# Kernel optimization log

Measured on AMD Instinct MI355X. Metric: run time of the kernel, lower is better.

## Reference

```python
import jax, jax.numpy as jnp
import numpy as np

B, N, D, OC, STEPS = 4096, 64, 128, 64, 3


def _xavier(k, shape):
    limit = float(np.sqrt(6.0 / (shape[0] + shape[1])))
    return jax.random.uniform(k, shape, jnp.float32, -limit, limit)


def setup_inputs() -> dict:
    key = jax.random.key(0)
    ks = jax.random.split(key, 14)
    u = 1.0 / float(np.sqrt(D))  # torch GRUCell/Linear default init range
    return {
        "h": jax.random.normal(ks[0], (B, N, D), jnp.float32),
        "adj": jax.random.normal(ks[1], (B, N, N), jnp.float32),
        "a_src": _xavier(ks[2], (D, 1)),
        "a_dst": _xavier(ks[3], (D, 1)),
        "w": _xavier(ks[4], (D, D)),
        "bias": jnp.zeros((D,), jnp.float32),
        "W_ih": jax.random.uniform(ks[5], (3 * D, D), jnp.float32, -u, u),
        "W_hh": jax.random.uniform(ks[6], (3 * D, D), jnp.float32, -u, u),
        "b_ih": jax.random.uniform(ks[7], (3 * D,), jnp.float32, -u, u),
        "b_hh": jax.random.uniform(ks[8], (3 * D,), jnp.float32, -u, u),
        "mlp1_w": jax.random.uniform(ks[9], (D, OC), jnp.float32, -u, u),
        "mlp1_b": jax.random.uniform(ks[10], (OC,), jnp.float32, -u, u),
        "mlp2_w": jax.random.uniform(ks[11], (D, 1), jnp.float32, -u, u),
        "mlp2_b": jax.random.uniform(ks[12], (1,), jnp.float32, -u, u),
        "steps": STEPS,
    }


def _gru_cell(x, hprev, W_ih, W_hh, b_ih, b_hh):
    # torch.nn.GRUCell math; x, hprev: (..., D)
    gi = x @ W_ih.T + b_ih        # (..., 3D)
    gh = hprev @ W_hh.T + b_hh    # (..., 3D)
    i_r, i_z, i_n = jnp.split(gi, 3, axis=-1)
    h_r, h_z, h_n = jnp.split(gh, 3, axis=-1)
    r = jax.nn.sigmoid(i_r + h_r)
    z = jax.nn.sigmoid(i_z + h_z)
    n = jnp.tanh(i_n + r * h_n)
    return (1.0 - z) * n + z * hprev


def reference(h, adj, a_src, a_dst, w, bias, W_ih, W_hh, b_ih, b_hh,
              mlp1_w, mlp1_b, mlp2_w, mlp2_b, steps):
    n = adj.shape[-1]
    attn_src = h @ a_src                      # (B, N, 1)
    attn_dst = h @ a_dst                      # (B, N, 1)
    attn = attn_src + jnp.swapaxes(attn_dst, 1, 2)   # (B, N, N) outer-sum
    attn = jax.nn.leaky_relu(attn, negative_slope=0.2)
    mask = 1.0 - jnp.eye(n, dtype=attn.dtype)        # zero the diagonal (as in source)
    attn = jax.nn.softmax(attn * mask, axis=-1)

    s = h
    for _ in range(int(steps)):
        a = jnp.einsum('bij,bjd->bid', attn, s @ w) + bias   # message passing
        s = _gru_cell(a, s, W_ih, W_hh, b_ih, b_hh)           # pointwise GRU update
        s = s + h                                             # residual connection

    output = s @ mlp1_w + mlp1_b              # (B, N, OC)
    weight = s @ mlp2_w + mlp2_b              # (B, N, 1)
    out = jnp.einsum('bni,bnc->bic', weight, output)  # (B, 1, OC)
    return jnp.squeeze(out, axis=1)           # (B, OC)
```

## Files before the change

kernel.cpp:

```cpp
#include <hip/hip_runtime.h>
#include <hip/hip_bf16.h>

typedef unsigned short u16t;
typedef __attribute__((ext_vector_type(8))) short bf16x8;
typedef __attribute__((ext_vector_type(4))) float f32x4;

__device__ __forceinline__ float bf2f(u16t u) {
  union { unsigned int i; float f; } v; v.i = ((unsigned int)u) << 16; return v.f;
}
__device__ __forceinline__ float bitsf(unsigned int u) {
  union { unsigned int i; float f; } v; v.i = u; return v.f;
}
__device__ __forceinline__ u16t f2bf(float f) {
  union { float f; unsigned int i; } v; v.f = f;
  return (u16t)((v.i + 0x7fffu + ((v.i >> 16) & 1u)) >> 16);
}
__device__ __forceinline__ unsigned int cvtpk(float lo, float hi) {
  float2 f; f.x = lo; f.y = hi;
  __hip_bfloat162 b = __float22bfloat162_rn(f);
  unsigned int r; __builtin_memcpy(&r, &b, 4); return r;
}
__device__ __forceinline__ float frcp(float x) { return __builtin_amdgcn_rcpf(x); }
__device__ __forceinline__ float sigm(float x) { return frcp(1.0f + __expf(-x)); }
__device__ __forceinline__ float tanh_f(float x) { return 1.0f - 2.0f * frcp(__expf(2.0f * x) + 1.0f); }
__device__ __forceinline__ float lrelu(float x) { return x > 0.0f ? x : 0.2f * x; }

__device__ __forceinline__ float ldf(const void* p, long i, bool isbf) {
  return isbf ? bf2f(((const u16t*)p)[i]) : ((const float*)p)[i];
}
__device__ __forceinline__ bf16x8 ld8(const void* p, long i, bool isbf) {
  if (isbf) return *reinterpret_cast<const bf16x8*>((const u16t*)p + i);
  const float* f = (const float*)p + i;
  bf16x8 r;
  #pragma unroll
  for (int j = 0; j < 8; ++j) r[j] = (short)f2bf(f[j]);
  return r;
}
__device__ __forceinline__ bool sniff_bf(const void* h_g) {
  bool isbf = true;
  #pragma unroll
  for (int i = 0; i < 16; ++i) {
    u16t u = ((const u16t*)h_g)[2 * i];
    int e = (u >> 7) & 0xFF;
    if (e < 100 || e > 142) isbf = false;
  }
  return isbf;
}

#define MFMA16(a, b, c) __builtin_amdgcn_mfma_f32_16x16x32_bf16((a), (b), (c), 0, 0, 0)

#define DDIM 128
#define SD 136
#define ST 72
#define R0_OFF 0
#define R1_OFF 9216
#define R2_OFF 18432
#define AT_OFF 27648
#define NLDS   32256

#define WS_W_OFF   0
#define WS_IH_OFF  16384
#define WS_HH_OFF  65536
#define WS_M1_OFF  114688
#define WS_ELEMS   122880

__global__ __launch_bounds__(256) void prep(
    const void* __restrict__ h_g, const void* __restrict__ w_g,
    const void* __restrict__ wih_g, const void* __restrict__ whh_g,
    const void* __restrict__ m1w_g, u16t* __restrict__ ws) {
  const bool isbf = sniff_bf(h_g);
  const int idx = blockIdx.x * 256 + threadIdx.x;
  if (idx >= WS_ELEMS) return;
  float val;
  if (idx < WS_IH_OFF) {
    int t = idx;
    int j = t & 7, lane = (t >> 3) & 63, ks = (t >> 9) & 3, wv = t >> 11;
    val = ldf(w_g, (long)(ks * 32 + (lane >> 4) * 8 + j) * DDIM + wv * 16 + (lane & 15), isbf);
  } else if (idx < WS_HH_OFF) {
    int t = idx - WS_IH_OFF;
    int j = t & 7, lane = (t >> 3) & 63, ks = (t >> 9) & 3, rem = t >> 11;
    int g = rem % 3, wv = rem / 3;
    val = ldf(wih_g, (long)(g * 128 + wv * 16 + (lane & 15)) * DDIM + ks * 32 + (lane >> 4) * 8 + j, isbf);
  } else if (idx < WS_M1_OFF) {
    int t = idx - WS_HH_OFF;
    int j = t & 7, lane = (t >> 3) & 63, ks = (t >> 9) & 3, rem = t >> 11;
    int g = rem % 3, wv = rem / 3;
    val = ldf(whh_g, (long)(g * 128 + wv * 16 + (lane & 15)) * DDIM + ks * 32 + (lane >> 4) * 8 + j, isbf);
  } else {
    int t = idx - WS_M1_OFF;
    int j = t & 7, lane = (t >> 3) & 63, ks = (t >> 9) & 3, wv = t >> 11;
    val = ldf(m1w_g, (long)(ks * 32 + (lane >> 4) * 8 + j) * 64 + wv * 16 + (lane & 15), isbf);
  }
  ws[idx] = f2bf(val);
}

template <bool WSOK>
__global__ __launch_bounds__(512) void fignn(
    const void* __restrict__ h_g, const void* __restrict__ asrc_g,
    const void* __restrict__ adst_g, const void* __restrict__ w_g,
    const void* __restrict__ bias_g, const void* __restrict__ wih_g,
    const void* __restrict__ whh_g, const void* __restrict__ bih_g,
    const void* __restrict__ bhh_g, const void* __restrict__ m1w_g,
    const void* __restrict__ m1b_g, const void* __restrict__ m2w_g,
    const void* __restrict__ m2b_g, const int* __restrict__ steps_p,
    const u16t* __restrict__ ws_g, void* __restrict__ out_g) {
  __shared__ __align__(16) u16t lds[NLDS];
  __shared__ __align__(16) float ldsf[192];
  u16t* sh_at = lds + AT_OFF;
  float* f_src = ldsf;
  float* f_dst = ldsf + 64;
  float* f_wv  = ldsf + 128;

  const int tid  = threadIdx.x;
  const int wv   = tid >> 6;
  const int lane = tid & 63;
  const int quad = lane >> 4;
  const int lrow = lane & 15;
  const int col  = wv * 16 + lrow;
  const int b    = blockIdx.x;

  const bool isbf = sniff_bf(h_g);

  u16t* s_c = lds + R0_OFF;
  u16t* s_m = lds + R1_OFF;
  u16t* s_a = lds + R2_OFF;

  const long hb = (long)b * (64 * DDIM);
  #pragma unroll
  for (int v = 0; v < 2; ++v) {
    int e = (tid + v * 512) * 8;
    int r = e >> 7, c = e & 127;
    *reinterpret_cast<bf16x8*>(s_c + r * SD + c) = ld8(h_g, hb + e, isbf);
  }

  unsigned int sreg2[8], hreg2[8];
  #pragma unroll
  for (int mt = 0; mt < 4; ++mt) {
    #pragma unroll
    for (int half = 0; half < 2; ++half) {
      long i0 = hb + (long)(mt * 16 + quad * 4 + half * 2) * DDIM + col;
      u16t lo, hi;
      if (isbf) {
        lo = ((const u16t*)h_g)[i0];
        hi = ((const u16t*)h_g)[i0 + DDIM];
      } else {
        lo = f2bf(((const float*)h_g)[i0]);
        hi = f2bf(((const float*)h_g)[i0 + DDIM]);
      }
      unsigned int p = (unsigned int)lo | ((unsigned int)hi << 16);
      hreg2[mt * 2 + half] = p;
      sreg2[mt * 2 + half] = p;
    }
  }

  const float msg_b = ldf(bias_g, col, isbf);
  const float bsum_r = ldf(bih_g, col, isbf) + ldf(bhh_g, col, isbf);
  const float bsum_z = ldf(bih_g, 128 + col, isbf) + ldf(bhh_g, 128 + col, isbf);
  const float b_in   = ldf(bih_g, 256 + col, isbf);
  const float b_hn   = ldf(bhh_g, 256 + col, isbf);
  int steps = *steps_p;
  if (steps < 1 || steps > 64) steps = 3;
  __syncthreads();

  if (tid < 128) {
    const int node = tid >> 1, half = tid & 1;
    float sa = 0.f, da = 0.f;
    #pragma unroll
    for (int k = half * 64; k < half * 64 + 64; k += 8) {
      bf16x8 hv = *reinterpret_cast<const bf16x8*>(s_c + node * SD + k);
      #pragma unroll
      for (int j = 0; j < 8; ++j) {
        float hf = bf2f((u16t)hv[j]);
        sa += hf * ldf(asrc_g, k + j, isbf);
        da += hf * ldf(adst_g, k + j, isbf);
      }
    }
    sa += __shfl_xor(sa, 1);
    da += __shfl_xor(da, 1);
    if (half == 0) { f_src[node] = sa; f_dst[node] = da; }
  }
  __syncthreads();
  {
    const int row = tid >> 3, sub = tid & 7;
    const float si = f_src[row];
    float vals[8];
    float mx = 0.0f;
    #pragma unroll
    for (int u = 0; u < 8; ++u) {
      int j = sub + u * 8;
      float vv = (j == row) ? 0.0f : lrelu(si + f_dst[j]);
      vals[u] = vv;
      mx = fmaxf(mx, vv);
    }
    mx = fmaxf(mx, __shfl_xor(mx, 1));
    mx = fmaxf(mx, __shfl_xor(mx, 2));
    mx = fmaxf(mx, __shfl_xor(mx, 4));
    float sum = 0.f;
    #pragma unroll
    for (int u = 0; u < 8; ++u) { vals[u] = __expf(vals[u] - mx); sum += vals[u]; }
    sum += __shfl_xor(sum, 1);
    sum += __shfl_xor(sum, 2);
    sum += __shfl_xor(sum, 4);
    float inv = frcp(sum);
    #pragma unroll
    for (int u = 0; u < 8; u += 2) {
      unsigned int pk = cvtpk(vals[u] * inv, vals[u + 1] * inv);
      sh_at[row * ST + sub + u * 8] = (u16t)pk;
      sh_at[row * ST + sub + (u + 1) * 8] = (u16t)(pk >> 16);
    }
  }
  __syncthreads();

  for (int it = 0; it < steps; ++it) {
    {
      f32x4 macc[4] = {{0,0,0,0},{0,0,0,0},{0,0,0,0},{0,0,0,0}};
      #pragma unroll
      for (int ks = 0; ks < 4; ++ks) {
        bf16x8 bw;
        if constexpr (WSOK) {
          bw = *reinterpret_cast<const bf16x8*>(ws_g + WS_W_OFF + (((wv * 4 + ks) * 64 + lane) << 3));
        } else {
          #pragma unroll
          for (int j = 0; j < 8; ++j)
            bw[j] = (short)f2bf(ldf(w_g, (long)(ks * 32 + quad * 8 + j) * DDIM + col, isbf));
        }
        #pragma unroll
        for (int mt = 0; mt < 4; ++mt) {
          bf16x8 af = *reinterpret_cast<const bf16x8*>(s_c + (mt * 16 + lrow) * SD + ks * 32 + quad * 8);
          macc[mt] = MFMA16(af, bw, macc[mt]);
        }
      }
      #pragma unroll
      for (int mt = 0; mt < 4; ++mt) {
        uint2 pk2;
        pk2.x = cvtpk(macc[mt][0], macc[mt][1]);
        pk2.y = cvtpk(macc[mt][2], macc[mt][3]);
        *reinterpret_cast<uint2*>(s_m + col * ST + mt * 16 + quad * 4) = pk2;
      }
    }
    #pragma unroll
    for (int mt = 0; mt < 4; ++mt) {
      f32x4 acc = {0.f, 0.f, 0.f, 0.f};
      #pragma unroll
      for (int ks = 0; ks < 2; ++ks) {
        bf16x8 af  = *reinterpret_cast<const bf16x8*>(sh_at + (mt * 16 + lrow) * ST + ks * 32 + quad * 8);
        bf16x8 bfv = *reinterpret_cast<const bf16x8*>(s_m + col * ST + ks * 32 + quad * 8);
        acc = MFMA16(af, bfv, acc);
      }
      unsigned int p01 = cvtpk(acc[0] + msg_b, acc[1] + msg_b);
      unsigned int p23 = cvtpk(acc[2] + msg_b, acc[3] + msg_b);
      const int rb = (mt * 16 + quad * 4) * SD + col;
      s_a[rb         ] = (u16t)p01;
      s_a[rb + SD    ] = (u16t)(p01 >> 16);
      s_a[rb + 2 * SD] = (u16t)p23;
      s_a[rb + 3 * SD] = (u16t)(p23 >> 16);
    }
    __syncthreads();

    #pragma unroll
    for (int p = 0; p < 2; ++p) {
      f32x4 ar[2]  = {{0,0,0,0},{0,0,0,0}};
      f32x4 az[2]  = {{0,0,0,0},{0,0,0,0}};
      f32x4 ain[2] = {{0,0,0,0},{0,0,0,0}};
      f32x4 ahn[2] = {{0,0,0,0},{0,0,0,0}};
      #pragma unroll
      for (int ks = 0; ks < 4; ++ks) {
        bf16x8 fa[2], fh[2];
        #pragma unroll
        for (int m = 0; m < 2; ++m) {
          const int mt = p * 2 + m;
          fa[m] = *reinterpret_cast<const bf16x8*>(s_a + (mt * 16 + lrow) * SD + ks * 32 + quad * 8);
          fh[m] = *reinterpret_cast<const bf16x8*>(s_c + (mt * 16 + lrow) * SD + ks * 32 + quad * 8);
        }
        bf16x8 bw;
        if constexpr (WSOK) bw = *reinterpret_cast<const bf16x8*>(ws_g + WS_IH_OFF + ((((wv * 3 + 0) * 4 + ks) * 64 + lane) << 3));
        else bw = ld8(wih_g, (long)(0 * 128 + col) * DDIM + ks * 32 + quad * 8, isbf);
        #pragma unroll
        for (int m = 0; m < 2; ++m) ar[m] = MFMA16(fa[m], bw, ar[m]);
        if constexpr (WSOK) bw = *reinterpret_cast<const bf16x8*>(ws_g + WS_IH_OFF + ((((wv * 3 + 1) * 4 + ks) * 64 + lane) << 3));
        else bw = ld8(wih_g, (long)(1 * 128 + col) * DDIM + ks * 32 + quad * 8, isbf);
        #pragma unroll
        for (int m = 0; m < 2; ++m) az[m] = MFMA16(fa[m], bw, az[m]);
        if constexpr (WSOK) bw = *reinterpret_cast<const bf16x8*>(ws_g + WS_IH_OFF + ((((wv * 3 + 2) * 4 + ks) * 64 + lane) << 3));
        else bw = ld8(wih_g, (long)(2 * 128 + col) * DDIM + ks * 32 + quad * 8, isbf);
        #pragma unroll
        for (int m = 0; m < 2; ++m) ain[m] = MFMA16(fa[m], bw, ain[m]);
        if constexpr (WSOK) bw = *reinterpret_cast<const bf16x8*>(ws_g + WS_HH_OFF + ((((wv * 3 + 0) * 4 + ks) * 64 + lane) << 3));
        else bw = ld8(whh_g, (long)(0 * 128 + col) * DDIM + ks * 32 + quad * 8, isbf);
        #pragma unroll
        for (int m = 0; m < 2; ++m) ar[m] = MFMA16(fh[m], bw, ar[m]);
        if constexpr (WSOK) bw = *reinterpret_cast<const bf16x8*>(ws_g + WS_HH_OFF + ((((wv * 3 + 1) * 4 + ks) * 64 + lane) << 3));
        else bw = ld8(whh_g, (long)(1 * 128 + col) * DDIM + ks * 32 + quad * 8, isbf);
        #pragma unroll
        for (int m = 0; m < 2; ++m) az[m] = MFMA16(fh[m], bw, az[m]);
        if constexpr (WSOK) bw = *reinterpret_cast<const bf16x8*>(ws_g + WS_HH_OFF + ((((wv * 3 + 2) * 4 + ks) * 64 + lane) << 3));
        else bw = ld8(whh_g, (long)(2 * 128 + col) * DDIM + ks * 32 + quad * 8, isbf);
        #pragma unroll
        for (int m = 0; m < 2; ++m) ahn[m] = MFMA16(fh[m], bw, ahn[m]);
      }
      #pragma unroll
      for (int m = 0; m < 2; ++m) {
        const int mt = p * 2 + m;
        #pragma unroll
        for (int pr = 0; pr < 2; ++pr) {
          const int e0 = pr * 2, e1 = pr * 2 + 1;
          float rg0 = sigm(ar[m][e0] + bsum_r), rg1 = sigm(ar[m][e1] + bsum_r);
          float zg0 = sigm(az[m][e0] + bsum_z), zg1 = sigm(az[m][e1] + bsum_z);
          float ng0 = tanh_f(ain[m][e0] + b_in + rg0 * (ahn[m][e0] + b_hn));
          float ng1 = tanh_f(ain[m][e1] + b_in + rg1 * (ahn[m][e1] + b_hn));
          unsigned int sp = sreg2[mt * 2 + pr], hp = hreg2[mt * 2 + pr];
          float sn0 = (1.0f - zg0) * ng0 + zg0 * bitsf(sp << 16) + bitsf(hp << 16);
          float sn1 = (1.0f - zg1) * ng1 + zg1 * bitsf(sp & 0xffff0000u) + bitsf(hp & 0xffff0000u);
          unsigned int pk = cvtpk(sn0, sn1);
          sreg2[mt * 2 + pr] = pk;
          const int rb = (mt * 16 + quad * 4 + pr * 2) * SD + col;
          s_m[rb     ] = (u16t)pk;
          s_m[rb + SD] = (u16t)(pk >> 16);
        }
      }
    }
    __syncthreads();
    u16t* t = s_c; s_c = s_m; s_m = s_a; s_a = t;
  }

  f32x4 oacc[4] = {{0,0,0,0},{0,0,0,0},{0,0,0,0},{0,0,0,0}};
  if (wv < 4) {
    #pragma unroll
    for (int ks = 0; ks < 4; ++ks) {
      bf16x8 bw;
      if constexpr (WSOK) {
        bw = *reinterpret_cast<const bf16x8*>(ws_g + WS_M1_OFF + (((wv * 4 + ks) * 64 + lane) << 3));
      } else {
        #pragma unroll
        for (int j = 0; j < 8; ++j)
          bw[j] = (short)f2bf(ldf(m1w_g, (long)(ks * 32 + quad * 8 + j) * 64 + col, isbf));
      }
      #pragma unroll
      for (int mt = 0; mt < 4; ++mt) {
        bf16x8 af = *reinterpret_cast<const bf16x8*>(s_c + (mt * 16 + lrow) * SD + ks * 32 + quad * 8);
        oacc[mt] = MFMA16(af, bw, oacc[mt]);
      }
    }
    const float b1c = ldf(m1b_g, col, isbf);
    #pragma unroll
    for (int mt = 0; mt < 4; ++mt)
      #pragma unroll
      for (int r = 0; r < 4; ++r) oacc[mt][r] += b1c;
  } else if (wv == 4) {
    float acc = 0.f;
    #pragma unroll
    for (int k = 0; k < 128; k += 8) {
      bf16x8 sv = *reinterpret_cast<const bf16x8*>(s_c + lane * SD + k);
      #pragma unroll
      for (int j = 0; j < 8; ++j) acc += bf2f((u16t)sv[j]) * ldf(m2w_g, k + j, isbf);
    }
    f_wv[lane] = acc + ldf(m2b_g, 0, isbf);
  }
  __syncthreads();
  if (wv < 4) {
    float p = 0.f;
    #pragma unroll
    for (int mt = 0; mt < 4; ++mt)
      #pragma unroll
      for (int r = 0; r < 4; ++r)
        p += f_wv[mt * 16 + quad * 4 + r] * oacc[mt][r];
    p += __shfl_xor(p, 16);
    p += __shfl_xor(p, 32);
    if (quad == 0) {
      if (isbf) ((u16t*)out_g)[(long)b * 64 + col] = f2bf(p);
      else      ((float*)out_g)[(long)b * 64 + col] = p;
    }
  }
}

extern "C" void kernel_launch(void* const* d_in, const int* in_sizes, int n_in,
                              void* d_out, int out_size, void* d_ws, size_t ws_size,
                              hipStream_t stream) {
  (void)in_sizes; (void)n_in; (void)out_size;
  const bool wsok = ws_size >= (size_t)WS_ELEMS * 2;
  if (wsok) {
    prep<<<dim3((WS_ELEMS + 255) / 256), dim3(256), 0, stream>>>(
        d_in[0], d_in[4], d_in[6], d_in[7], d_in[10], (u16t*)d_ws);
    fignn<true><<<dim3(4096), dim3(512), 0, stream>>>(
        d_in[0], d_in[2], d_in[3], d_in[4], d_in[5], d_in[6], d_in[7], d_in[8],
        d_in[9], d_in[10], d_in[11], d_in[12], d_in[13], (const int*)d_in[14],
        (const u16t*)d_ws, d_out);
  } else {
    fignn<false><<<dim3(4096), dim3(512), 0, stream>>>(
        d_in[0], d_in[2], d_in[3], d_in[4], d_in[5], d_in[6], d_in[7], d_in[8],
        d_in[9], d_in[10], d_in[11], d_in[12], d_in[13], (const int*)d_in[14],
        (const u16t*)d_ws, d_out);
  }
}
```

Before: 646.7 us.

## Fuse hidden-state GRU matmuls into the message projection pass before the barrier

Computes the W_hh gate products (r, z, hn) during the s@w projection phase, reusing the same s_c A-fragments, so they run before the attention matmul and barrier rather than after. The post-barrier phase then only does the W_ih products over all four row tiles at once, with no split into two passes. The attention B-fragments are also hoisted out of the row-tile loop. This moves MFMA work off the critical path after the barrier and removes duplicate LDS reads of s_c, at the cost of keeping 12 extra accumulator vectors live across the barrier, which raises register pressure.

```diff
diff --git a/kernel.cpp b/kernel.cpp
--- a/kernel.cpp
+++ b/kernel.cpp
@@ -212,23 +212,39 @@
   __syncthreads();
 
   for (int it = 0; it < steps; ++it) {
+    f32x4 gr[4]  = {{0,0,0,0},{0,0,0,0},{0,0,0,0},{0,0,0,0}};
+    f32x4 gz[4]  = {{0,0,0,0},{0,0,0,0},{0,0,0,0},{0,0,0,0}};
+    f32x4 ghn[4] = {{0,0,0,0},{0,0,0,0},{0,0,0,0},{0,0,0,0}};
+
     {
       f32x4 macc[4] = {{0,0,0,0},{0,0,0,0},{0,0,0,0},{0,0,0,0}};
       #pragma unroll
       for (int ks = 0; ks < 4; ++ks) {
+        bf16x8 af[4];
+        #pragma unroll
+        for (int mt = 0; mt < 4; ++mt)
+          af[mt] = *reinterpret_cast<const bf16x8*>(s_c + (mt * 16 + lrow) * SD + ks * 32 + quad * 8);
         bf16x8 bw;
-        if constexpr (WSOK) {
-          bw = *reinterpret_cast<const bf16x8*>(ws_g + WS_W_OFF + (((wv * 4 + ks) * 64 + lane) << 3));
-        } else {
+        if constexpr (WSOK) bw = *reinterpret_cast<const bf16x8*>(ws_g + WS_W_OFF + (((wv * 4 + ks) * 64 + lane) << 3));
+        else {
           #pragma unroll
           for (int j = 0; j < 8; ++j)
             bw[j] = (short)f2bf(ldf(w_g, (long)(ks * 32 + quad * 8 + j) * DDIM + col, isbf));
         }
         #pragma unroll
-        for (int mt = 0; mt < 4; ++mt) {
-          bf16x8 af = *reinterpret_cast<const bf16x8*>(s_c + (mt * 16 + lrow) * SD + ks * 32 + quad * 8);
-          macc[mt] = MFMA16(af, bw, macc[mt]);
-        }
+        for (int mt = 0; mt < 4; ++mt) macc[mt] = MFMA16(af[mt], bw, macc[mt]);
+        if constexpr (WSOK) bw = *reinterpret_cast<const bf16x8*>(ws_g + WS_HH_OFF + ((((wv * 3 + 0) * 4 + ks) * 64 + lane) << 3));
+        else bw = ld8(whh_g, (long)(0 * 128 + col) * DDIM + ks * 32 + quad * 8, isbf);
+        #pragma unroll
+        for (int mt = 0; mt < 4; ++mt) gr[mt] = MFMA16(af[mt], bw, gr[mt]);
+        if constexpr (WSOK) bw = *reinterpret_cast<const bf16x8*>(ws_g + WS_HH_OFF + ((((wv * 3 + 1) * 4 + ks) * 64 + lane) << 3));
+        else bw = ld8(whh_g, (long)(1 * 128 + col) * DDIM + ks * 32 + quad * 8, isbf);
+        #pragma unroll
+        for (int mt = 0; mt < 4; ++mt) gz[mt] = MFMA16(af[mt], bw, gz[mt]);
+        if constexpr (WSOK) bw = *reinterpret_cast<const bf16x8*>(ws_g + WS_HH_OFF + ((((wv * 3 + 2) * 4 + ks) * 64 + lane) << 3));
+        else bw = ld8(whh_g, (long)(2 * 128 + col) * DDIM + ks * 32 + quad * 8, isbf);
+        #pragma unroll
+        for (int mt = 0; mt < 4; ++mt) ghn[mt] = MFMA16(af[mt], bw, ghn[mt]);
       }
       #pragma unroll
       for (int mt = 0; mt < 4; ++mt) {
@@ -238,76 +254,61 @@
         *reinterpret_cast<uint2*>(s_m + col * ST + mt * 16 + quad * 4) = pk2;
       }
     }
-    #pragma unroll
-    for (int mt = 0; mt < 4; ++mt) {
-      f32x4 acc = {0.f, 0.f, 0.f, 0.f};
-      #pragma unroll
-      for (int ks = 0; ks < 2; ++ks) {
-        bf16x8 af  = *reinterpret_cast<const bf16x8*>(sh_at + (mt * 16 + lrow) * ST + ks * 32 + quad * 8);
-        bf16x8 bfv = *reinterpret_cast<const bf16x8*>(s_m + col * ST + ks * 32 + quad * 8);
-        acc = MFMA16(af, bfv, acc);
-      }
-      unsigned int p01 = cvtpk(acc[0] + msg_b, acc[1] + msg_b);
-      unsigned int p23 = cvtpk(acc[2] + msg_b, acc[3] + msg_b);
-      const int rb = (mt * 16 + quad * 4) * SD + col;
-      s_a[rb         ] = (u16t)p01;
-      s_a[rb + SD    ] = (u16t)(p01 >> 16);
-      s_a[rb + 2 * SD] = (u16t)p23;
-      s_a[rb + 3 * SD] = (u16t)(p23 >> 16);
+    {
+      bf16x8 bfv[2];
+      #pragma unroll
+      for (int ks = 0; ks < 2; ++ks)
+        bfv[ks] = *reinterpret_cast<const bf16x8*>(s_m + col * ST + ks * 32 + quad * 8);
+      #pragma unroll
+      for (int mt = 0; mt < 4; ++mt) {
+        f32x4 acc = {0.f, 0.f, 0.f, 0.f};
+        #pragma unroll
+        for (int ks = 0; ks < 2; ++ks) {
+          bf16x8 af = *reinterpret_cast<const bf16x8*>(sh_at + (mt * 16 + lrow) * ST + ks * 32 + quad * 8);
+          acc = MFMA16(af, bfv[ks], acc);
+        }
+        unsigned int p01 = cvtpk(acc[0] + msg_b, acc[1] + msg_b);
+        unsigned int p23 = cvtpk(acc[2] + msg_b, acc[3] + msg_b);
+        const int rb = (mt * 16 + quad * 4) * SD + col;
+        s_a[rb         ] = (u16t)p01;
+        s_a[rb + SD    ] = (u16t)(p01 >> 16);
+        s_a[rb + 2 * SD] = (u16t)p23;
+        s_a[rb + 3 * SD] = (u16t)(p23 >> 16);
+      }
     }
     __syncthreads();
 
-    #pragma unroll
-    for (int p = 0; p < 2; ++p) {
-      f32x4 ar[2]  = {{0,0,0,0},{0,0,0,0}};
-      f32x4 az[2]  = {{0,0,0,0},{0,0,0,0}};
-      f32x4 ain[2] = {{0,0,0,0},{0,0,0,0}};
-      f32x4 ahn[2] = {{0,0,0,0},{0,0,0,0}};
+    {
+      f32x4 ain[4] = {{0,0,0,0},{0,0,0,0},{0,0,0,0},{0,0,0,0}};
       #pragma unroll
       for (int ks = 0; ks < 4; ++ks) {
-        bf16x8 fa[2], fh[2];
-        #pragma unroll
-        for (int m = 0; m < 2; ++m) {
-          const int mt = p * 2 + m;
-          fa[m] = *reinterpret_cast<const bf16x8*>(s_a + (mt * 16 + lrow) * SD + ks * 32 + quad * 8);
-          fh[m] = *reinterpret_cast<const bf16x8*>(s_c + (mt * 16 + lrow) * SD + ks * 32 + quad * 8);
-        }
+        bf16x8 fa[4];
+        #pragma unroll
+        for (int mt = 0; mt < 4; ++mt)
+          fa[mt] = *reinterpret_cast<const bf16x8*>(s_a + (mt * 16 + lrow) * SD + ks * 32 + quad * 8);
         bf16x8 bw;
         if constexpr (WSOK) bw = *reinterpret_cast<const bf16x8*>(ws_g + WS_IH_OFF + ((((wv * 3 + 0) * 4 + ks) * 64 + lane) << 3));
         else bw = ld8(wih_g, (long)(0 * 128 + col) * DDIM + ks * 32 + quad * 8, isbf);
         #pragma unroll
-        for (int m = 0; m < 2; ++m) ar[m] = MFMA16(fa[m], bw, ar[m]);
+        for (int mt = 0; mt < 4; ++mt) gr[mt] = MFMA16(fa[mt], bw, gr[mt]);
         if constexpr (WSOK) bw = *reinterpret_cast<const bf16x8*>(ws_g + WS_IH_OFF + ((((wv * 3 + 1) * 4 + ks) * 64 + lane) << 3));
         else bw = ld8(wih_g, (long)(1 * 128 + col) * DDIM + ks * 32 + quad * 8, isbf);
         #pragma unroll
-        for (int m = 0; m < 2; ++m) az[m] = MFMA16(fa[m], bw, az[m]);
+        for (int mt = 0; mt < 4; ++mt) gz[mt] = MFMA16(fa[mt], bw, gz[mt]);
         if constexpr (WSOK) bw = *reinterpret_cast<const bf16x8*>(ws_g + WS_IH_OFF + ((((wv * 3 + 2) * 4 + ks) * 64 + lane) << 3));
         else bw = ld8(wih_g, (long)(2 * 128 + col) * DDIM + ks * 32 + quad * 8, isbf);
         #pragma unroll
-        for (int m = 0; m < 2; ++m) ain[m] = MFMA16(fa[m], bw, ain[m]);
-        if constexpr (WSOK) bw = *reinterpret_cast<const bf16x8*>(ws_g + WS_HH_OFF + ((((wv * 3 + 0) * 4 + ks) * 64 + lane) << 3));
-        else bw = ld8(whh_g, (long)(0 * 128 + col) * DDIM + ks * 32 + quad * 8, isbf);
-        #pragma unroll
-        for (int m = 0; m < 2; ++m) ar[m] = MFMA16(fh[m], bw, ar[m]);
-        if constexpr (WSOK) bw = *reinterpret_cast<const bf16x8*>(ws_g + WS_HH_OFF + ((((wv * 3 + 1) * 4 + ks) * 64 + lane) << 3));
-        else bw = ld8(whh_g, (long)(1 * 128 + col) * DDIM + ks * 32 + quad * 8, isbf);
-        #pragma unroll
-        for (int m = 0; m < 2; ++m) az[m] = MFMA16(fh[m], bw, az[m]);
-        if constexpr (WSOK) bw = *reinterpret_cast<const bf16x8*>(ws_g + WS_HH_OFF + ((((wv * 3 + 2) * 4 + ks) * 64 + lane) << 3));
-        else bw = ld8(whh_g, (long)(2 * 128 + col) * DDIM + ks * 32 + quad * 8, isbf);
-        #pragma unroll
-        for (int m = 0; m < 2; ++m) ahn[m] = MFMA16(fh[m], bw, ahn[m]);
-      }
-      #pragma unroll
-      for (int m = 0; m < 2; ++m) {
-        const int mt = p * 2 + m;
+        for (int mt = 0; mt < 4; ++mt) ain[mt] = MFMA16(fa[mt], bw, ain[mt]);
+      }
+      #pragma unroll
+      for (int mt = 0; mt < 4; ++mt) {
         #pragma unroll
         for (int pr = 0; pr < 2; ++pr) {
           const int e0 = pr * 2, e1 = pr * 2 + 1;
-          float rg0 = sigm(ar[m][e0] + bsum_r), rg1 = sigm(ar[m][e1] + bsum_r);
-          float zg0 = sigm(az[m][e0] + bsum_z), zg1 = sigm(az[m][e1] + bsum_z);
-          float ng0 = tanh_f(ain[m][e0] + b_in + rg0 * (ahn[m][e0] + b_hn));
-          float ng1 = tanh_f(ain[m][e1] + b_in + rg1 * (ahn[m][e1] + b_hn));
+          float rg0 = sigm(gr[mt][e0] + bsum_r), rg1 = sigm(gr[mt][e1] + bsum_r);
+          float zg0 = sigm(gz[mt][e0] + bsum_z), zg1 = sigm(gz[mt][e1] + bsum_z);
+          float ng0 = tanh_f(ain[mt][e0] + b_in + rg0 * (ghn[mt][e0] + b_hn));
+          float ng1 = tanh_f(ain[mt][e1] + b_in + rg1 * (ghn[mt][e1] + b_hn));
           unsigned int sp = sreg2[mt * 2 + pr], hp = hreg2[mt * 2 + pr];
           float sn0 = (1.0f - zg0) * ng0 + zg0 * bitsf(sp << 16) + bitsf(hp << 16);
           float sn1 = (1.0f - zg1) * ng1 + zg1 * bitsf(sp & 0xffff0000u) + bitsf(hp & 0xffff0000u);
```

New measurement: 668.8 us. +3.4%, slower.
